# Performance work log

Measured on AMD Instinct MI355X. Metric: run time of the kernel, lower is better.

The kernel has to match this reference:

```python
import jax, jax.numpy as jnp
import numpy as np

B, T, S, L, R, H, UE = 64, 256, 16, 128, 16, 256, 64


def setup_inputs() -> dict:
    key = jax.random.key(0)
    ks = jax.random.split(key, 10)
    u = jax.random.normal(ks[0], (B, T, UE), jnp.float32)
    k = 0.1 * jax.random.normal(ks[1], (B, T, L), jnp.float32)
    K = 0.1 * jax.random.normal(ks[2], (B, T, L, R), jnp.float32)
    eps_z = jax.random.normal(ks[3], (T, S, B, L), jnp.float32)
    eps_w = jax.random.normal(ks[4], (T, S, B, R), jnp.float32)
    W1 = jax.random.normal(ks[5], (L, H), jnp.float32) / np.sqrt(L).astype(np.float32)
    W2 = jax.random.normal(ks[6], (H, L), jnp.float32) / np.sqrt(H).astype(np.float32)
    m_init = jax.random.normal(ks[7], (L,), jnp.float32)
    Q_diag = jax.random.uniform(ks[8], (L,), jnp.float32, 0.1, 1.0)
    Q0_diag = jax.random.uniform(ks[9], (L,), jnp.float32, 0.5, 1.5)
    return dict(u=u, k=k, K=K, eps_z=eps_z, eps_w=eps_w, W1=W1, W2=W2,
                m_init=m_init, Q_diag=Q_diag, Q0_diag=Q0_diag, n_samples=S)


def reference(u, k, K, eps_z, eps_w, W1, W2, m_init, Q_diag, Q0_diag, n_samples):
    Bn, Tn, Ln, Rn = K.shape
    ue = u.shape[-1]
    I_r = jnp.eye(Rn, dtype=K.dtype)

    def bmv(A, x):      # A: [B,L,R], x: [...,B,R] -> [...,B,L]
        return jnp.einsum('blr,...br->...bl', A, x)

    def bmvT(A, x):     # A: [B,L,R], x: [...,B,L] -> [...,B,R]
        return jnp.einsum('blr,...bl->...br', A, x)

    def mean_fn(z):
        return z + jnp.tanh(z @ W1) @ W2

    def step_core(m, K_t, k_t, ez, ew, q_a):
        # A = I + K^T diag(q_a) K  (rank x rank)
        A = I_r + jnp.einsum('blr,l,blq->brq', K_t, q_a, K_t)
        Lc = jnp.linalg.cholesky(A)
        Linv = jax.scipy.linalg.solve_triangular(
            Lc, jnp.broadcast_to(I_r, Lc.shape), lower=True)

        def csolve(x):  # solve A y = x via Linv^T Linv x
            y = jnp.einsum('bij,...bj->...bi', Linv, x)
            return jnp.einsum('bji,...bj->...bi', Linv, y)

        # gain direction; inner shift always uses Q_diag (as in torch source)
        g = k_t - bmv(K_t, csolve(bmvT(K_t, m + Q_diag * k_t)))
        m_f = m + q_a * g
        z_p = jnp.sqrt(q_a) * ez
        z_f = m_f + z_p - bmv(K_t, csolve(bmvT(K_t, z_p) + ew))
        qp = jnp.sum(q_a * g * g, axis=-1)
        M = A - I_r  # = K^T diag(q_a) K
        tr = -jnp.einsum('bij,bjk,bik->b', Linv, M, Linv)
        logdet = 2.0 * jnp.sum(jnp.log(jnp.diagonal(Lc, axis1=-2, axis2=-1)), axis=-1)
        kl = 0.5 * (qp + tr + logdet)
        return z_f, m_f, z_p, kl

    # ---- t = 0 (uses initial covariance Q0_diag) ----
    m0 = jnp.broadcast_to(m_init, (Bn, Ln))
    m0 = m0.at[:, :ue].add(u[:, 0])
    z_f0, m_f0, z_p0, kl0 = step_core(m0, K[:, 0], k[:, 0], eps_z[0], eps_w[0], Q0_diag)

    # ---- t = 1..T-1: sequential nonlinear filter scan ----
    def scan_fn(z_prev, xs):
        u_t, k_t, K_t, ez, ew = xs
        m = mean_fn(z_prev)            # [S,B,L]
        m = m.at[..., :ue].add(u_t)    # broadcast input over samples
        z_f, m_f, z_p, kl = step_core(m, K_t, k_t, ez, ew, Q_diag)
        return z_f, (z_f, m_f.mean(axis=0), z_p, kl.mean(axis=0))

    xs = (jnp.swapaxes(u[:, 1:], 0, 1),
          jnp.swapaxes(k[:, 1:], 0, 1),
          jnp.swapaxes(K[:, 1:], 0, 1),
          eps_z[1:], eps_w[1:])
    _, (z_fs, m_fs, z_ps, kls) = jax.lax.scan(scan_fn, z_f0, xs)

    z_f = jnp.transpose(jnp.concatenate([z_f0[None], z_fs], 0), (1, 2, 0, 3))  # [S,B,T,L]
    m_f = jnp.transpose(jnp.concatenate([m_f0[None], m_fs], 0), (1, 0, 2))     # [B,T,L]
    z_p = jnp.transpose(jnp.concatenate([z_p0[None], z_ps], 0), (1, 2, 0, 3))  # [S,B,T,L]
    kl = jnp.concatenate([kl0[None], kls], 0).T                                 # [B,T]
    return z_f, m_f, z_p, kl
```

## Files before the change

### kernel.cpp

```cpp
#include <hip/hip_runtime.h>
#include <cstddef>

typedef _Float16 half8v __attribute__((ext_vector_type(8)));
typedef _Float16 half4v __attribute__((ext_vector_type(4)));
typedef float f32x4 __attribute__((ext_vector_type(4)));

#define MFMA32(A, B, C) __builtin_amdgcn_mfma_f32_16x16x32_f16(A, B, C, 0, 0, 0)
#define MFMA16(A, B, C) __builtin_amdgcn_mfma_f32_16x16x16f16(A, B, C, 0, 0, 0)

__global__ void kw2_kernel(const float* __restrict__ W2, _Float16* __restrict__ w2h) {
  int i = blockIdx.x * 256 + threadIdx.x;
  w2h[i] = (_Float16)W2[i];
}

__global__ void kprep1_kernel(const float* __restrict__ Kg,
                              const float* __restrict__ kg,
                              const float* __restrict__ ug,
                              const float* __restrict__ Qd,
                              const float* __restrict__ Q0d,
                              float* __restrict__ Ainv,
                              float* __restrict__ klc,
                              _Float16* __restrict__ pfb,
                              float* __restrict__ cgp) {
  int tid = threadIdx.x;
  int wv = tid >> 6, ln = tid & 63;
  size_t bt = (size_t)blockIdx.x * 4 + wv;
  int t = (int)(bt & 255);
  __shared__ float Ks[4][128][20];
  __shared__ float qs[4][128];
  __shared__ float vvs[4][128];
  __shared__ float Asm[4][16][20];
  __shared__ float LiL[4][16][20];
  __shared__ float AiS[4][16][20];
  __shared__ float yps[4][4][16];
  __shared__ float yvs[4][16];

  const float* kp = Kg + bt * 2048;
  for (int i = ln; i < 2048; i += 64) Ks[wv][i >> 4][i & 15] = kp[i];
  for (int l = ln; l < 128; l += 64) {
    float q = (t == 0) ? Q0d[l] : Qd[l];
    qs[wv][l] = q;
    float v = Qd[l] * kg[bt * 128 + l];
    if (t > 0 && l < 64) v += ug[bt * 64 + l];
    vvs[wv][l] = v;
  }
  __syncthreads();
  {
    int r = ln & 15, c0 = (ln >> 4) << 2;
    float a0 = 0, a1 = 0, a2 = 0, a3 = 0;
    for (int l = 0; l < 128; ++l) {
      float kq = Ks[wv][l][r] * qs[wv][l];
      const float* row = &Ks[wv][l][c0];
      a0 += kq * row[0]; a1 += kq * row[1]; a2 += kq * row[2]; a3 += kq * row[3];
    }
    Asm[wv][r][c0 + 0] = a0 + ((r == c0 + 0) ? 1.f : 0.f);
    Asm[wv][r][c0 + 1] = a1 + ((r == c0 + 1) ? 1.f : 0.f);
    Asm[wv][r][c0 + 2] = a2 + ((r == c0 + 2) ? 1.f : 0.f);
    Asm[wv][r][c0 + 3] = a3 + ((r == c0 + 3) ? 1.f : 0.f);
  }
  {
    int r = ln & 15, seg = ln >> 4;
    float s = 0.f;
    for (int l = seg * 32; l < seg * 32 + 32; ++l) s += Ks[wv][l][r] * vvs[wv][l];
    yps[wv][seg][r] = s;
  }
  __syncthreads();
  if (ln < 16) {
    int i = ln;
    float ar[16], Lr[16];
#pragma unroll
    for (int j = 0; j < 16; ++j) ar[j] = Asm[wv][i][j];
    float ld = 0.f;
#pragma unroll
    for (int j = 0; j < 16; ++j) {
      float ajj = __shfl(ar[j], j, 64);
      float d = sqrtf(ajj);
      ld += __logf(d);
      float li = ar[j] / d;
      li = (i >= j) ? li : 0.f;
      Lr[j] = li;
#pragma unroll
      for (int k2 = j; k2 < 16; ++k2) {
        float lk = __shfl(li, k2, 64);
        ar[k2] -= li * lk;
      }
    }
    int cc = i;
    float Lic[16];
#pragma unroll
    for (int ii = 0; ii < 16; ++ii) {
      float s = (ii == cc) ? 1.f : 0.f;
#pragma unroll
      for (int p = 0; p < 16; ++p) {
        if (p < ii) {
          float Lip = __shfl(Lr[p], ii, 64);
          s -= Lip * Lic[p];
        }
      }
      float dii = __shfl(Lr[ii], ii, 64);
      float v = s / dii;
      Lic[ii] = (ii >= cc) ? v : 0.f;
    }
    float tr = 0.f;
#pragma unroll
    for (int ii = 0; ii < 16; ++ii) { tr += Lic[ii] * Lic[ii]; LiL[wv][cc][ii] = Lic[ii]; }
    tr += __shfl_xor(tr, 1); tr += __shfl_xor(tr, 2);
    tr += __shfl_xor(tr, 4); tr += __shfl_xor(tr, 8);
    if (cc == 0) klc[bt] = 0.5f * (tr - 16.f + 2.f * ld);
    yvs[wv][cc] = yps[wv][0][cc] + yps[wv][1][cc] + yps[wv][2][cc] + yps[wv][3][cc];
  }
  __syncthreads();
  {
    int r = ln & 15, c0 = (ln >> 4) << 2;
    float a0 = 0, a1 = 0, a2 = 0, a3 = 0;
    for (int ii = 0; ii < 16; ++ii) {
      float lir = LiL[wv][r][ii];
      a0 += lir * LiL[wv][c0 + 0][ii];
      a1 += lir * LiL[wv][c0 + 1][ii];
      a2 += lir * LiL[wv][c0 + 2][ii];
      a3 += lir * LiL[wv][c0 + 3][ii];
    }
    AiS[wv][r][c0 + 0] = a0; AiS[wv][r][c0 + 1] = a1;
    AiS[wv][r][c0 + 2] = a2; AiS[wv][r][c0 + 3] = a3;
    f32x4 av = {a0, a1, a2, a3};
    *(f32x4*)&Ainv[bt * 256 + r * 16 + c0] = av;
  }
  __syncthreads();
  {
#pragma unroll
    for (int li = 0; li < 2; ++li) {
      int l = ln * 2 + li;
      f32x4 acc0 = {0,0,0,0}, acc1v = {0,0,0,0}, acc2v = {0,0,0,0}, acc3v = {0,0,0,0};
      for (int j = 0; j < 16; ++j) {
        float kj = Ks[wv][l][j];
        acc0  += kj * *(const f32x4*)&AiS[wv][j][0];
        acc1v += kj * *(const f32x4*)&AiS[wv][j][4];
        acc2v += kj * *(const f32x4*)&AiS[wv][j][8];
        acc3v += kj * *(const f32x4*)&AiS[wv][j][12];
      }
      float ql = qs[wv][l];
      float cp = ql * kg[bt * 128 + l];
      float pv[16];
#pragma unroll
      for (int e = 0; e < 4; ++e) {
        pv[e] = ql * acc0[e]; pv[4 + e] = ql * acc1v[e];
        pv[8 + e] = ql * acc2v[e]; pv[12 + e] = ql * acc3v[e];
      }
#pragma unroll
      for (int r = 0; r < 16; ++r) cp -= pv[r] * yvs[wv][r];
      cgp[bt * 128 + l] = cp;
#pragma unroll
      for (int r = 0; r < 16; ++r) Ks[wv][l][r] = pv[r];
    }
  }
  __syncthreads();
  {
    int gp = ln >> 4, cp = ln & 15;
#pragma unroll
    for (int ci = 0; ci < 4; ++ci) {
      half8v o;
#pragma unroll
      for (int mt = 0; mt < 2; ++mt)
#pragma unroll
        for (int j = 0; j < 4; ++j)
          o[mt * 4 + j] = (_Float16)Ks[wv][ci * 32 + mt * 16 + cp][gp * 4 + j];
      *(half8v*)(pfb + bt * 2048 + (size_t)(ci * 64 + ln) * 8) = o;
    }
  }
}

__global__ void kprepR_kernel(const float* __restrict__ Kg,
                              const _Float16* __restrict__ w2h,
                              _Float16* __restrict__ rfb,
                              _Float16* __restrict__ kab) {
  int tid = threadIdx.x;
  int wv = tid >> 6, ln = tid & 63;
  int g = ln >> 4, c = ln & 15;
  __shared__ _Float16 Kh[128][20];
  __shared__ _Float16 Rh[16][264];
  for (int it = 0; it < 4; ++it) {
    size_t bt = (size_t)blockIdx.x * 4 + it;
    const float* kp = Kg + bt * 2048;
    for (int i = tid; i < 2048; i += 256) Kh[i >> 4][i & 15] = (_Float16)kp[i];
    __syncthreads();
    half8v kA[4];
#pragma unroll
    for (int kt = 0; kt < 4; ++kt)
#pragma unroll
      for (int j = 0; j < 8; ++j) kA[kt][j] = Kh[kt * 32 + g * 8 + j][c];
#pragma unroll
    for (int i = 0; i < 4; ++i) {
      int tile = wv * 4 + i;
      f32x4 acc = {0, 0, 0, 0};
#pragma unroll
      for (int kt = 0; kt < 4; ++kt) {
        half8v bf = *(const half8v*)&w2h[(size_t)(tile * 16 + c) * 128 + kt * 32 + g * 8];
        acc = MFMA32(kA[kt], bf, acc);
      }
#pragma unroll
      for (int r = 0; r < 4; ++r) Rh[g * 4 + r][tile * 16 + c] = (_Float16)acc[r];
    }
    __syncthreads();
    half8v r0, r1;
#pragma unroll
    for (int mt = 0; mt < 4; ++mt)
#pragma unroll
      for (int j = 0; j < 4; ++j) {
        _Float16 v = Rh[c][wv * 64 + mt * 16 + g * 4 + j];
        if (mt < 2) r0[mt * 4 + j] = v; else r1[(mt - 2) * 4 + j] = v;
      }
    *(half8v*)(rfb + bt * 4096 + (size_t)tid * 16) = r0;
    *(half8v*)(rfb + bt * 4096 + (size_t)tid * 16 + 8) = r1;
    if (kab) {
      half8v ko;
#pragma unroll
      for (int kt = 0; kt < 2; ++kt)
#pragma unroll
        for (int j = 0; j < 4; ++j) ko[kt * 4 + j] = Kh[wv * 32 + kt * 16 + g * 4 + j][c];
      *(half8v*)(kab + bt * 2048 + (size_t)tid * 8) = ko;
    }
    __syncthreads();
  }
}

__global__ void kc_kernel(const float* __restrict__ Kg,
                          const float* __restrict__ epsz,
                          const float* __restrict__ epsw,
                          const float* __restrict__ Qd,
                          const float* __restrict__ Q0d,
                          const float* __restrict__ Ainv,
                          float* __restrict__ out_zf,
                          float* __restrict__ out_zp,
                          float* __restrict__ zpcb,
                          int zw, int wzp) {
  int idx = blockIdx.x;
  int t = idx >> 6, b = idx & 63;
  int bt = b * 256 + t;
  __shared__ float Ks[128][16];
  __shared__ float Ai[16][16];
  __shared__ float zp[16][129];
  __shared__ float hh[16][17];
  __shared__ float ww[16][17];
  __shared__ float sq[128];
  const float* kp = Kg + (size_t)bt * 2048;
  for (int i = threadIdx.x; i < 2048; i += 256) ((float*)Ks)[i] = kp[i];
  ((float*)Ai)[threadIdx.x] = Ainv[(size_t)bt * 256 + threadIdx.x];
  const float* q = (t == 0) ? Q0d : Qd;
  if (threadIdx.x < 128) sq[threadIdx.x] = sqrtf(q[threadIdx.x]);
  __syncthreads();
  for (int i = threadIdx.x; i < 2048; i += 256) {
    int s = i >> 7, l = i & 127;
    float v = sq[l] * epsz[(((size_t)t * 16 + s) * 64 + b) * 128 + l];
    zp[s][l] = v;
    if (wzp) out_zp[(((size_t)s * 64 + b) * 256 + t) * 128 + l] = v;
  }
  __syncthreads();
  {
    int s = threadIdx.x >> 4, r = threadIdx.x & 15;
    float acc = epsw[(((size_t)t * 16 + s) * 64 + b) * 16 + r];
    for (int l = 0; l < 128; ++l) acc += Ks[l][r] * zp[s][l];
    hh[s][r] = acc;
  }
  __syncthreads();
  {
    int s = threadIdx.x >> 4, r = threadIdx.x & 15;
    float acc = 0.f;
    for (int j = 0; j < 16; ++j) acc += Ai[r][j] * hh[s][j];
    ww[s][r] = acc;
  }
  __syncthreads();
  for (int i = threadIdx.x; i < 2048; i += 256) {
    int s = i >> 7, l = i & 127;
    float acc = 0.f;
    for (int r = 0; r < 16; ++r) acc += Ks[l][r] * ww[s][r];
    float v = zp[s][l] - acc;
    if (zw) zpcb[(size_t)bt * 2048 + i] = v;
    else out_zf[(((size_t)s * 64 + b) * 256 + t) * 128 + l] = v;
  }
}

__global__ void kzp_kernel(const float* __restrict__ epsz,
                           const float* __restrict__ Qd,
                           const float* __restrict__ Q0d,
                           float* __restrict__ out_zp) {
  for (size_t i = (size_t)blockIdx.x * blockDim.x + threadIdx.x; i < (size_t)33554432;
       i += (size_t)gridDim.x * blockDim.x) {
    int l = (int)(i & 127);
    int t = (int)((i >> 7) & 255);
    int sb = (int)(i >> 15);
    int s = sb >> 6, b = sb & 63;
    float q = (t == 0) ? Q0d[l] : Qd[l];
    out_zp[i] = sqrtf(q) * epsz[(((size_t)t * 16 + s) * 64 + b) * 128 + l];
  }
}

#define BAR() asm volatile("s_waitcnt lgkmcnt(0)\n\ts_barrier" ::: "memory")

template <bool PK, bool ZW>
__device__ __forceinline__ void scan_body(
    const int b, const int ct,
    _Float16* __restrict__ svhc, _Float16* __restrict__ hbc,
    float (*__restrict__ h2pc)[320], float (*__restrict__ qppc)[64],
    const float* __restrict__ ug, const float* __restrict__ Kg,
    const float* __restrict__ W1, const float* __restrict__ W2,
    const float* __restrict__ m_init, const float* __restrict__ Qd,
    const float* __restrict__ Q0d, const _Float16* __restrict__ pfb,
    const float* __restrict__ cgp, const _Float16* __restrict__ rfb,
    const _Float16* __restrict__ kab, const float* __restrict__ zpcb,
    const float* __restrict__ klcp, float* __restrict__ out_zf,
    float* __restrict__ out_mf, float* __restrict__ out_kl) {
  const int wvc = ct >> 6;
  const int ln = ct & 63;
  const int g = ln >> 4;
  const int c = ln & 15;

  half8v w1f[4][4];
#pragma unroll
  for (int mt = 0; mt < 4; ++mt)
#pragma unroll
    for (int kt = 0; kt < 4; ++kt) {
      half8v v;
#pragma unroll
      for (int j = 0; j < 8; ++j)
        v[j] = (_Float16)W1[(size_t)(kt * 32 + g * 8 + j) * 256 + (wvc * 64 + mt * 16 + c)];
      w1f[mt][kt] = v;
    }
  half8v w2f[2][8];
#pragma unroll
  for (int mt = 0; mt < 2; ++mt)
#pragma unroll
    for (int kt = 0; kt < 8; ++kt) {
      half8v v;
#pragma unroll
      for (int j = 0; j < 8; ++j)
        v[j] = (_Float16)W2[(size_t)(kt * 32 + g * 8 + j) * 128 + (wvc * 32 + mt * 16 + c)];
      w2f[mt][kt] = v;
    }

  f32x4 qiv[2], qiv0[2];
#pragma unroll
  for (int mt = 0; mt < 2; ++mt) {
    f32x4 q = *(const f32x4*)&Qd[wvc * 32 + mt * 16 + g * 4];
    f32x4 q0 = *(const f32x4*)&Q0d[wvc * 32 + mt * 16 + g * 4];
#pragma unroll
    for (int r = 0; r < 4; ++r) { qiv[mt][r] = 1.f / q[r]; qiv0[mt][r] = 1.f / q0[r]; }
  }

  f32x4 zreg[2];

  half8v pfx0, pfx1, kax0 = {}, kax1 = {}, rfa0, rfa1, rfc0, rfc1;
  float kf0[8], kf1[8];
  f32x4 zq0[2], zq1[2], cv0[2], cv1[2];
  f32x4 ur0[2] = {}, ur1[2] = {};
  float kv0 = 0.f, kv1 = 0.f;

  const char* pf_p = (const char*)pfb + (size_t)b * 256 * 4096 + (size_t)ct * 16;
  const char* ka_p = PK ? (const char*)kab + (size_t)b * 256 * 4096 + (size_t)ct * 16
                        : (const char*)pfb;
  const char* K_p = (const char*)Kg + (size_t)b * 256 * 8192 + (size_t)((wvc * 32 + g * 4) * 16 + c) * 4;
  const char* rf_p = (const char*)rfb + (size_t)b * 256 * 8192 + (size_t)ct * 32;
  const char* zq_p = ZW ? (const char*)zpcb + (size_t)b * 256 * 8192 + (size_t)(c * 128 + wvc * 32 + g * 4) * 4
                        : (const char*)out_zf + ((((size_t)c * 64 + b) * 256) * 128 + wvc * 32 + g * 4) * 4;
  const size_t zq_str = ZW ? 8192 : 512;
  const char* cv_p = (const char*)cgp + (size_t)b * 256 * 512 + (size_t)(wvc * 32 + g * 4) * 4;
  const char* ur_p = (const char*)ug + (size_t)b * 256 * 256 + (size_t)(wvc * 32 + g * 4) * 4;
  const char* kl_p = (const char*)klcp + (size_t)b * 256 * 4;
  char* zf_p = (char*)out_zf + ((((size_t)c * 64 + b) * 256) * 128 + wvc * 32 + g * 4) * 4;
  char* mf_p = (char*)out_mf + ((size_t)b * 256 * 128 + wvc * 32 + g * 4) * 4;

#define STAGE(BI) do { \
    pfx##BI = *(const half8v*)pf_p; pf_p += 4096; \
    if constexpr (PK) { kax##BI = *(const half8v*)ka_p; ka_p += 4096; } \
    else { _Pragma("unroll") for (int kt_ = 0; kt_ < 2; ++kt_) \
             _Pragma("unroll") for (int j_ = 0; j_ < 4; ++j_) \
               kf##BI[kt_ * 4 + j_] = *(const float*)(K_p + kt_ * 1024 + j_ * 64); \
           K_p += 8192; } \
    rfa##BI = *(const half8v*)rf_p; rfc##BI = *(const half8v*)(rf_p + 16); rf_p += 8192; \
    zq##BI[0] = *(const f32x4*)zq_p; zq##BI[1] = *(const f32x4*)(zq_p + 64); zq_p += zq_str; \
    cv##BI[0] = *(const f32x4*)cv_p; cv##BI[1] = *(const f32x4*)(cv_p + 64); cv_p += 512; \
    if (wvc < 2) { ur##BI[0] = *(const f32x4*)ur_p; ur##BI[1] = *(const f32x4*)(ur_p + 64); } \
    ur_p += 256; \
    kv##BI = *(const float*)kl_p; kl_p += 4; \
  } while (0)

#define KAH(BI, KT, DST) do { \
    if constexpr (PK) { _Pragma("unroll") for (int j_ = 0; j_ < 4; ++j_) DST[j_] = kax##BI[(KT) * 4 + j_]; } \
    else { _Pragma("unroll") for (int j_ = 0; j_ < 4; ++j_) DST[j_] = (_Float16)kf##BI[(KT) * 4 + j_]; } \
  } while (0)

#define PHASE_A(BI) do { \
    half4v zbh_[2], zbl_[2]; \
    _Pragma("unroll") for (int kt = 0; kt < 2; ++kt) \
      _Pragma("unroll") for (int j = 0; j < 4; ++j) { \
        float x_ = zreg[kt][j]; _Float16 h_ = (_Float16)x_; \
        zbh_[kt][j] = h_; zbl_[kt][j] = (_Float16)(x_ - (float)h_); } \
    half8v zh8_[4]; \
    _Pragma("unroll") for (int kt = 0; kt < 4; ++kt) { \
      int row_ = kt * 4 + g; \
      int idx_ = row_ * 128 + (((c + row_) & 15) << 3); \
      zh8_[kt] = *(const half8v*)&svhc[idx_]; } \
    f32x4 a1h_[4]; \
    _Pragma("unroll") for (int mt = 0; mt < 4; ++mt) a1h_[mt] = (f32x4){0,0,0,0}; \
    _Pragma("unroll") for (int kt = 0; kt < 4; ++kt) \
      _Pragma("unroll") for (int mt = 0; mt < 4; ++mt) \
        a1h_[mt] = MFMA32(w1f[mt][kt], zh8_[kt], a1h_[mt]); \
    half4v th_[4]; \
    _Pragma("unroll") for (int mt = 0; mt < 4; ++mt) { \
      _Pragma("unroll") for (int r = 0; r < 4; ++r) { \
        float x_ = a1h_[mt][r]; \
        float e_ = __expf(2.f * x_); \
        th_[mt][r] = (_Float16)(1.f - 2.f / (e_ + 1.f)); } \
      int row_ = wvc * 8 + mt * 2 + (g >> 1); \
      *(half4v*)&hbc[row_ * 128 + (((c + row_) & 15) << 3) + ((g & 1) << 2)] = th_[mt]; } \
    half4v ka0_, ka1_; KAH(BI, 0, ka0_); KAH(BI, 1, ka1_); \
    f32x4 hz_ = {0, 0, 0, 0}; \
    hz_ = MFMA16(ka0_, zbh_[0], hz_); hz_ = MFMA16(ka1_, zbh_[1], hz_); \
    hz_ = MFMA16(ka0_, zbl_[0], hz_); hz_ = MFMA16(ka1_, zbl_[1], hz_); \
    f32x4 hr_ = {0, 0, 0, 0}; \
    _Pragma("unroll") for (int mt = 0; mt < 4; ++mt) { \
      half4v rr_; \
      _Pragma("unroll") for (int j = 0; j < 4; ++j) \
        rr_[j] = (mt < 2) ? rfa##BI[mt * 4 + j] : rfc##BI[(mt - 2) * 4 + j]; \
      hr_ = MFMA16(rr_, th_[mt], hr_); } \
    *(f32x4*)&h2pc[wvc][c * 20 + g * 4] = hz_ + hr_; \
  } while (0)

#define EPILOG(BI, QIV, MV) do { \
    f32x4 h2v_ = *(const f32x4*)&h2pc[0][c * 20 + g * 4]; \
    h2v_ += *(const f32x4*)&h2pc[1][c * 20 + g * 4]; \
    h2v_ += *(const f32x4*)&h2pc[2][c * 20 + g * 4]; \
    h2v_ += *(const f32x4*)&h2pc[3][c * 20 + g * 4]; \
    half4v h2h_, h2l_; \
    _Pragma("unroll") for (int j = 0; j < 4; ++j) { \
      _Float16 h_ = (_Float16)h2v_[j]; \
      h2h_[j] = h_; h2l_[j] = (_Float16)(h2v_[j] - (float)h_); } \
    float qpl_ = 0.f; \
    _Pragma("unroll") for (int mt = 0; mt < 2; ++mt) { \
      half4v pfm_; \
      _Pragma("unroll") for (int j = 0; j < 4; ++j) pfm_[j] = pfx##BI[mt * 4 + j]; \
      f32x4 zz_ = {0, 0, 0, 0}; \
      f32x4 mh_ = MFMA16(pfm_, h2h_, zz_); \
      f32x4 mlv_ = MFMA16(pfm_, h2l_, zz_); \
      f32x4 dd_ = cv##BI[mt] - (mh_ + mlv_); \
      f32x4 mf_ = MV[mt] + dd_; \
      f32x4 zf_ = mf_ + zq##BI[mt]; \
      _Pragma("unroll") for (int r = 0; r < 4; ++r) qpl_ += dd_[r] * dd_[r] * QIV[mt][r]; \
      *(f32x4*)(zf_p + mt * 64) = zf_; \
      zreg[mt] = zf_; \
      half4v zh4_; \
      _Pragma("unroll") for (int r = 0; r < 4; ++r) zh4_[r] = (_Float16)zf_[r]; \
      int row_ = wvc * 4 + mt * 2 + (g >> 1); \
      int base_ = row_ * 128 + (((c + row_) & 15) << 3) + ((g & 1) << 2); \
      *(half4v*)&svhc[base_] = zh4_; \
      f32x4 ms_ = mf_; \
      _Pragma("unroll") for (int r = 0; r < 4; ++r) { \
        float x_ = ms_[r]; \
        x_ += __shfl_xor(x_, 1); x_ += __shfl_xor(x_, 2); \
        x_ += __shfl_xor(x_, 4); x_ += __shfl_xor(x_, 8); \
        ms_[r] = x_ * 0.0625f; } \
      if (c == 0) *(f32x4*)(mf_p + mt * 64) = ms_; \
    } \
    zf_p += 512; mf_p += 512; \
    qpl_ += __shfl_xor(qpl_, 16); \
    qpl_ += __shfl_xor(qpl_, 32); \
    if (g == 0) qppc[BI][wvc * 16 + c] = qpl_; \
  } while (0)

#define PHASE_B(BI, QIV) do { \
    half8v hf_[8]; \
    _Pragma("unroll") for (int kt = 0; kt < 8; ++kt) { \
      int row_ = kt * 4 + g; \
      hf_[kt] = *(const half8v*)&hbc[row_ * 128 + (((c + row_) & 15) << 3)]; } \
    f32x4 a2a_[2], a2b_[2]; \
    _Pragma("unroll") for (int mt = 0; mt < 2; ++mt) { a2a_[mt] = (f32x4){0,0,0,0}; a2b_[mt] = (f32x4){0,0,0,0}; } \
    _Pragma("unroll") for (int kt = 0; kt < 4; ++kt) \
      _Pragma("unroll") for (int mt = 0; mt < 2; ++mt) { \
        a2a_[mt] = MFMA32(w2f[mt][kt], hf_[kt], a2a_[mt]); \
        a2b_[mt] = MFMA32(w2f[mt][kt + 4], hf_[kt + 4], a2b_[mt]); } \
    f32x4 mv_[2]; \
    _Pragma("unroll") for (int mt = 0; mt < 2; ++mt) { \
      mv_[mt] = zreg[mt] + a2a_[mt] + a2b_[mt]; \
      if (wvc < 2) mv_[mt] += ur##BI[mt]; } \
    EPILOG(BI, QIV, mv_); \
  } while (0)

#define KL_FIN(PBI, TPREV) do { \
    if (ct < 16) { \
      float v_ = qppc[PBI][ct] + qppc[PBI][16 + ct] + qppc[PBI][32 + ct] + qppc[PBI][48 + ct]; \
      v_ += __shfl_xor(v_, 1); v_ += __shfl_xor(v_, 2); \
      v_ += __shfl_xor(v_, 4); v_ += __shfl_xor(v_, 8); \
      if (ct == 0) out_kl[(size_t)b * 256 + (size_t)(TPREV)] = 0.03125f * v_ + kv##PBI; \
    } \
  } while (0)

  STAGE(0);
  STAGE(1);
  {
    f32x4 mv0[2];
#pragma unroll
    for (int mt = 0; mt < 2; ++mt) {
      mv0[mt] = *(const f32x4*)&m_init[wvc * 32 + mt * 16 + g * 4];
      if (wvc < 2) mv0[mt] += ur0[mt];
    }
    half4v mh0[2], ml0[2];
#pragma unroll
    for (int kt = 0; kt < 2; ++kt)
#pragma unroll
      for (int j = 0; j < 4; ++j) {
        float x = mv0[kt][j];
        _Float16 h = (_Float16)x;
        mh0[kt][j] = h;
        ml0[kt][j] = (_Float16)(x - (float)h);
      }
    half4v ka0_, ka1_;
    KAH(0, 0, ka0_); KAH(0, 1, ka1_);
    f32x4 hz = {0, 0, 0, 0};
    hz = MFMA16(ka0_, mh0[0], hz); hz = MFMA16(ka1_, mh0[1], hz);
    hz = MFMA16(ka0_, ml0[0], hz); hz = MFMA16(ka1_, ml0[1], hz);
    *(f32x4*)&h2pc[wvc][c * 20 + g * 4] = hz;
    BAR();
    EPILOG(0, qiv0, mv0);
    BAR();
  }

  for (int t = 1; t < 255; t += 2) {
    KL_FIN(0, t - 1);
    STAGE(0);
    PHASE_A(1);
    BAR();
    PHASE_B(1, qiv);
    BAR();
    KL_FIN(1, t);
    STAGE(1);
    PHASE_A(0);
    BAR();
    PHASE_B(0, qiv);
    BAR();
  }
  KL_FIN(0, 254);
  PHASE_A(1);
  BAR();
  PHASE_B(1, qiv);
  BAR();
  KL_FIN(1, 255);

#undef STAGE
#undef KAH
#undef PHASE_A
#undef EPILOG
#undef PHASE_B
#undef KL_FIN
}

template <bool PK, bool ZW>
__launch_bounds__(256, 1)
__global__ void kscan1_kernel(const float* __restrict__ ug, const float* __restrict__ Kg,
                              const float* __restrict__ W1, const float* __restrict__ W2,
                              const float* __restrict__ m_init, const float* __restrict__ Qd,
                              const float* __restrict__ Q0d, const _Float16* __restrict__ pfb,
                              const float* __restrict__ cgp, const _Float16* __restrict__ rfb,
                              const _Float16* __restrict__ kab, const float* __restrict__ zpcb,
                              const float* __restrict__ klcp, float* __restrict__ out_zf,
                              float* __restrict__ out_mf, float* __restrict__ out_kl) {
  __shared__ __align__(16) _Float16 svh[2048];
  __shared__ __align__(16) _Float16 hb[4096];
  __shared__ float h2p[4][320];
  __shared__ float qpp[2][64];
  scan_body<PK, ZW>(blockIdx.x, threadIdx.x, svh, hb, h2p, qpp,
                    ug, Kg, W1, W2, m_init, Qd, Q0d, pfb, cgp, rfb, kab, zpcb, klcp,
                    out_zf, out_mf, out_kl);
}

template <bool PK, bool ZW>
__attribute__((amdgpu_flat_work_group_size(512, 512)))
__attribute__((amdgpu_waves_per_eu(2, 2)))
__global__ void kscan2_kernel(const float* __restrict__ ug, const float* __restrict__ Kg,
                              const float* __restrict__ W1, const float* __restrict__ W2,
                              const float* __restrict__ m_init, const float* __restrict__ Qd,
                              const float* __restrict__ Q0d, const _Float16* __restrict__ pfb,
                              const float* __restrict__ cgp, const _Float16* __restrict__ rfb,
                              const _Float16* __restrict__ kab, const float* __restrict__ zpcb,
                              const float* __restrict__ klcp, float* __restrict__ out_zf,
                              float* __restrict__ out_mf, float* __restrict__ out_kl) {
  __shared__ __align__(16) _Float16 svh[2][2048];
  __shared__ __align__(16) _Float16 hb[2][4096];
  __shared__ float h2p[2][4][320];
  __shared__ float qpp[2][2][64];
  const int ch = threadIdx.x >> 8;
  scan_body<PK, ZW>(blockIdx.x * 2 + ch, threadIdx.x & 255,
                    svh[ch], hb[ch], h2p[ch], qpp[ch],
                    ug, Kg, W1, W2, m_init, Qd, Q0d, pfb, cgp, rfb, kab, zpcb, klcp,
                    out_zf, out_mf, out_kl);
}

extern "C" void kernel_launch(void* const* d_in, const int* in_sizes, int n_in,
                              void* d_out, int out_size, void* d_ws, size_t ws_size,
                              hipStream_t stream) {
  (void)in_sizes; (void)n_in; (void)out_size;
  const float* u   = (const float*)d_in[0];
  const float* kk  = (const float*)d_in[1];
  const float* Kg  = (const float*)d_in[2];
  const float* epz = (const float*)d_in[3];
  const float* epw = (const float*)d_in[4];
  const float* W1  = (const float*)d_in[5];
  const float* W2  = (const float*)d_in[6];
  const float* mi  = (const float*)d_in[7];
  const float* Qd  = (const float*)d_in[8];
  const float* Q0d = (const float*)d_in[9];

  float* out_zf = (float*)d_out;
  float* out_mf = out_zf + (size_t)33554432;
  float* out_zp = out_mf + (size_t)2097152;
  float* out_kl = out_zp + (size_t)33554432;

  char* ws = (char*)d_ws;
  size_t off = 0;
  auto take = [&](size_t n) { char* p = ws + off; off += n; return p; };
  float*    Ainv = (float*)take(16777216);
  float*    klc  = (float*)take(65536);
  float*    cgp  = (float*)take(8388608);
  _Float16* pfb  = (_Float16*)take(67108864);
  _Float16* w2h  = (_Float16*)take(65536);
  bool zw = ws_size >= off + 134217728;
  float* zpcb = zw ? (float*)take(134217728) : nullptr;
  bool pk = zw && (ws_size >= off + 67108864);
  _Float16* kab = pk ? (_Float16*)take(67108864) : nullptr;
  bool rfws = ws_size >= off + 134217728;
  _Float16* rfb = rfws ? (_Float16*)take(134217728) : (_Float16*)out_zp;
  int wzp = rfws ? 1 : 0;

  kw2_kernel<<<128, 256, 0, stream>>>(W2, w2h);
  kprep1_kernel<<<4096, 256, 0, stream>>>(Kg, kk, u, Qd, Q0d, Ainv, klc, pfb, cgp);
  kprepR_kernel<<<4096, 256, 0, stream>>>(Kg, w2h, rfb, kab);
  kc_kernel<<<16384, 256, 0, stream>>>(Kg, epz, epw, Qd, Q0d, Ainv, out_zf, out_zp,
                                       zpcb, zw ? 1 : 0, wzp);

  auto pick = [&](const void* f2) {
    hipFuncAttributes fa;
    if (hipFuncGetAttributes(&fa, f2) == hipSuccess)
      return fa.localSizeBytes == 0 && fa.numRegs > 140;
    return false;
  };
#define LAUNCH_SCAN(PKV, ZWV) do { \
    if (pick((const void*)kscan2_kernel<PKV, ZWV>)) \
      kscan2_kernel<PKV, ZWV><<<32, 512, 0, stream>>>(u, Kg, W1, W2, mi, Qd, Q0d, pfb, cgp, rfb, kab, zpcb, klc, out_zf, out_mf, out_kl); \
    else \
      kscan1_kernel<PKV, ZWV><<<64, 256, 0, stream>>>(u, Kg, W1, W2, mi, Qd, Q0d, pfb, cgp, rfb, kab, zpcb, klc, out_zf, out_mf, out_kl); \
  } while (0)

  if (pk)      LAUNCH_SCAN(true,  true);
  else if (zw) LAUNCH_SCAN(false, true);
  else         LAUNCH_SCAN(false, false);
#undef LAUNCH_SCAN

  if (!rfws) kzp_kernel<<<2048, 256, 0, stream>>>(epz, Qd, Q0d, out_zp);
}
```

Measured before the change: 1.078 ms.

## Fuse prep stages and scan into one persistent kernel with per-timestep flags

Merges the precompute kernels (Cholesky/inverse, W2 projection, noise correction, z_p output) into a single launch. In it, 64 blocks run the sequential scan while 192 worker blocks produce per-(b,t) data and signal readiness through global flags. Scan blocks spin on acquire loads before consuming each timestep, so preprocessing overlaps the latency-bound scan instead of running before it. This relies on all 256 blocks being co-resident, since otherwise the spin-waits could deadlock. It also drops the two-chain-per-block scan variant.

```diff
diff --git a/kernel.cpp b/kernel.cpp
--- a/kernel.cpp
+++ b/kernel.cpp
@@ -11,287 +11,6 @@
 __global__ void kw2_kernel(const float* __restrict__ W2, _Float16* __restrict__ w2h) {
   int i = blockIdx.x * 256 + threadIdx.x;
   w2h[i] = (_Float16)W2[i];
-}
-
-__global__ void kprep1_kernel(const float* __restrict__ Kg,
-                              const float* __restrict__ kg,
-                              const float* __restrict__ ug,
-                              const float* __restrict__ Qd,
-                              const float* __restrict__ Q0d,
-                              float* __restrict__ Ainv,
-                              float* __restrict__ klc,
-                              _Float16* __restrict__ pfb,
-                              float* __restrict__ cgp) {
-  int tid = threadIdx.x;
-  int wv = tid >> 6, ln = tid & 63;
-  size_t bt = (size_t)blockIdx.x * 4 + wv;
-  int t = (int)(bt & 255);
-  __shared__ float Ks[4][128][20];
-  __shared__ float qs[4][128];
-  __shared__ float vvs[4][128];
-  __shared__ float Asm[4][16][20];
-  __shared__ float LiL[4][16][20];
-  __shared__ float AiS[4][16][20];
-  __shared__ float yps[4][4][16];
-  __shared__ float yvs[4][16];
-
-  const float* kp = Kg + bt * 2048;
-  for (int i = ln; i < 2048; i += 64) Ks[wv][i >> 4][i & 15] = kp[i];
-  for (int l = ln; l < 128; l += 64) {
-    float q = (t == 0) ? Q0d[l] : Qd[l];
-    qs[wv][l] = q;
-    float v = Qd[l] * kg[bt * 128 + l];
-    if (t > 0 && l < 64) v += ug[bt * 64 + l];
-    vvs[wv][l] = v;
-  }
-  __syncthreads();
-  {
-    int r = ln & 15, c0 = (ln >> 4) << 2;
-    float a0 = 0, a1 = 0, a2 = 0, a3 = 0;
-    for (int l = 0; l < 128; ++l) {
-      float kq = Ks[wv][l][r] * qs[wv][l];
-      const float* row = &Ks[wv][l][c0];
-      a0 += kq * row[0]; a1 += kq * row[1]; a2 += kq * row[2]; a3 += kq * row[3];
-    }
-    Asm[wv][r][c0 + 0] = a0 + ((r == c0 + 0) ? 1.f : 0.f);
-    Asm[wv][r][c0 + 1] = a1 + ((r == c0 + 1) ? 1.f : 0.f);
-    Asm[wv][r][c0 + 2] = a2 + ((r == c0 + 2) ? 1.f : 0.f);
-    Asm[wv][r][c0 + 3] = a3 + ((r == c0 + 3) ? 1.f : 0.f);
-  }
-  {
-    int r = ln & 15, seg = ln >> 4;
-    float s = 0.f;
-    for (int l = seg * 32; l < seg * 32 + 32; ++l) s += Ks[wv][l][r] * vvs[wv][l];
-    yps[wv][seg][r] = s;
-  }
-  __syncthreads();
-  if (ln < 16) {
-    int i = ln;
-    float ar[16], Lr[16];
-#pragma unroll
-    for (int j = 0; j < 16; ++j) ar[j] = Asm[wv][i][j];
-    float ld = 0.f;
-#pragma unroll
-    for (int j = 0; j < 16; ++j) {
-      float ajj = __shfl(ar[j], j, 64);
-      float d = sqrtf(ajj);
-      ld += __logf(d);
-      float li = ar[j] / d;
-      li = (i >= j) ? li : 0.f;
-      Lr[j] = li;
-#pragma unroll
-      for (int k2 = j; k2 < 16; ++k2) {
-        float lk = __shfl(li, k2, 64);
-        ar[k2] -= li * lk;
-      }
-    }
-    int cc = i;
-    float Lic[16];
-#pragma unroll
-    for (int ii = 0; ii < 16; ++ii) {
-      float s = (ii == cc) ? 1.f : 0.f;
-#pragma unroll
-      for (int p = 0; p < 16; ++p) {
-        if (p < ii) {
-          float Lip = __shfl(Lr[p], ii, 64);
-          s -= Lip * Lic[p];
-        }
-      }
-      float dii = __shfl(Lr[ii], ii, 64);
-      float v = s / dii;
-      Lic[ii] = (ii >= cc) ? v : 0.f;
-    }
-    float tr = 0.f;
-#pragma unroll
-    for (int ii = 0; ii < 16; ++ii) { tr += Lic[ii] * Lic[ii]; LiL[wv][cc][ii] = Lic[ii]; }
-    tr += __shfl_xor(tr, 1); tr += __shfl_xor(tr, 2);
-    tr += __shfl_xor(tr, 4); tr += __shfl_xor(tr, 8);
-    if (cc == 0) klc[bt] = 0.5f * (tr - 16.f + 2.f * ld);
-    yvs[wv][cc] = yps[wv][0][cc] + yps[wv][1][cc] + yps[wv][2][cc] + yps[wv][3][cc];
-  }
-  __syncthreads();
-  {
-    int r = ln & 15, c0 = (ln >> 4) << 2;
-    float a0 = 0, a1 = 0, a2 = 0, a3 = 0;
-    for (int ii = 0; ii < 16; ++ii) {
-      float lir = LiL[wv][r][ii];
-      a0 += lir * LiL[wv][c0 + 0][ii];
-      a1 += lir * LiL[wv][c0 + 1][ii];
-      a2 += lir * LiL[wv][c0 + 2][ii];
-      a3 += lir * LiL[wv][c0 + 3][ii];
-    }
-    AiS[wv][r][c0 + 0] = a0; AiS[wv][r][c0 + 1] = a1;
-    AiS[wv][r][c0 + 2] = a2; AiS[wv][r][c0 + 3] = a3;
-    f32x4 av = {a0, a1, a2, a3};
-    *(f32x4*)&Ainv[bt * 256 + r * 16 + c0] = av;
-  }
-  __syncthreads();
-  {
-#pragma unroll
-    for (int li = 0; li < 2; ++li) {
-      int l = ln * 2 + li;
-      f32x4 acc0 = {0,0,0,0}, acc1v = {0,0,0,0}, acc2v = {0,0,0,0}, acc3v = {0,0,0,0};
-      for (int j = 0; j < 16; ++j) {
-        float kj = Ks[wv][l][j];
-        acc0  += kj * *(const f32x4*)&AiS[wv][j][0];
-        acc1v += kj * *(const f32x4*)&AiS[wv][j][4];
-        acc2v += kj * *(const f32x4*)&AiS[wv][j][8];
-        acc3v += kj * *(const f32x4*)&AiS[wv][j][12];
-      }
-      float ql = qs[wv][l];
-      float cp = ql * kg[bt * 128 + l];
-      float pv[16];
-#pragma unroll
-      for (int e = 0; e < 4; ++e) {
-        pv[e] = ql * acc0[e]; pv[4 + e] = ql * acc1v[e];
-        pv[8 + e] = ql * acc2v[e]; pv[12 + e] = ql * acc3v[e];
-      }
-#pragma unroll
-      for (int r = 0; r < 16; ++r) cp -= pv[r] * yvs[wv][r];
-      cgp[bt * 128 + l] = cp;
-#pragma unroll
-      for (int r = 0; r < 16; ++r) Ks[wv][l][r] = pv[r];
-    }
-  }
-  __syncthreads();
-  {
-    int gp = ln >> 4, cp = ln & 15;
-#pragma unroll
-    for (int ci = 0; ci < 4; ++ci) {
-      half8v o;
-#pragma unroll
-      for (int mt = 0; mt < 2; ++mt)
-#pragma unroll
-        for (int j = 0; j < 4; ++j)
-          o[mt * 4 + j] = (_Float16)Ks[wv][ci * 32 + mt * 16 + cp][gp * 4 + j];
-      *(half8v*)(pfb + bt * 2048 + (size_t)(ci * 64 + ln) * 8) = o;
-    }
-  }
-}
-
-__global__ void kprepR_kernel(const float* __restrict__ Kg,
-                              const _Float16* __restrict__ w2h,
-                              _Float16* __restrict__ rfb,
-                              _Float16* __restrict__ kab) {
-  int tid = threadIdx.x;
-  int wv = tid >> 6, ln = tid & 63;
-  int g = ln >> 4, c = ln & 15;
-  __shared__ _Float16 Kh[128][20];
-  __shared__ _Float16 Rh[16][264];
-  for (int it = 0; it < 4; ++it) {
-    size_t bt = (size_t)blockIdx.x * 4 + it;
-    const float* kp = Kg + bt * 2048;
-    for (int i = tid; i < 2048; i += 256) Kh[i >> 4][i & 15] = (_Float16)kp[i];
-    __syncthreads();
-    half8v kA[4];
-#pragma unroll
-    for (int kt = 0; kt < 4; ++kt)
-#pragma unroll
-      for (int j = 0; j < 8; ++j) kA[kt][j] = Kh[kt * 32 + g * 8 + j][c];
-#pragma unroll
-    for (int i = 0; i < 4; ++i) {
-      int tile = wv * 4 + i;
-      f32x4 acc = {0, 0, 0, 0};
-#pragma unroll
-      for (int kt = 0; kt < 4; ++kt) {
-        half8v bf = *(const half8v*)&w2h[(size_t)(tile * 16 + c) * 128 + kt * 32 + g * 8];
-        acc = MFMA32(kA[kt], bf, acc);
-      }
-#pragma unroll
-      for (int r = 0; r < 4; ++r) Rh[g * 4 + r][tile * 16 + c] = (_Float16)acc[r];
-    }
-    __syncthreads();
-    half8v r0, r1;
-#pragma unroll
-    for (int mt = 0; mt < 4; ++mt)
-#pragma unroll
-      for (int j = 0; j < 4; ++j) {
-        _Float16 v = Rh[c][wv * 64 + mt * 16 + g * 4 + j];
-        if (mt < 2) r0[mt * 4 + j] = v; else r1[(mt - 2) * 4 + j] = v;
-      }
-    *(half8v*)(rfb + bt * 4096 + (size_t)tid * 16) = r0;
-    *(half8v*)(rfb + bt * 4096 + (size_t)tid * 16 + 8) = r1;
-    if (kab) {
-      half8v ko;
-#pragma unroll
-      for (int kt = 0; kt < 2; ++kt)
-#pragma unroll
-        for (int j = 0; j < 4; ++j) ko[kt * 4 + j] = Kh[wv * 32 + kt * 16 + g * 4 + j][c];
-      *(half8v*)(kab + bt * 2048 + (size_t)tid * 8) = ko;
-    }
-    __syncthreads();
-  }
-}
-
-__global__ void kc_kernel(const float* __restrict__ Kg,
-                          const float* __restrict__ epsz,
-                          const float* __restrict__ epsw,
-                          const float* __restrict__ Qd,
-                          const float* __restrict__ Q0d,
-                          const float* __restrict__ Ainv,
-                          float* __restrict__ out_zf,
-                          float* __restrict__ out_zp,
-                          float* __restrict__ zpcb,
-                          int zw, int wzp) {
-  int idx = blockIdx.x;
-  int t = idx >> 6, b = idx & 63;
-  int bt = b * 256 + t;
-  __shared__ float Ks[128][16];
-  __shared__ float Ai[16][16];
-  __shared__ float zp[16][129];
-  __shared__ float hh[16][17];
-  __shared__ float ww[16][17];
-  __shared__ float sq[128];
-  const float* kp = Kg + (size_t)bt * 2048;
-  for (int i = threadIdx.x; i < 2048; i += 256) ((float*)Ks)[i] = kp[i];
-  ((float*)Ai)[threadIdx.x] = Ainv[(size_t)bt * 256 + threadIdx.x];
-  const float* q = (t == 0) ? Q0d : Qd;
-  if (threadIdx.x < 128) sq[threadIdx.x] = sqrtf(q[threadIdx.x]);
-  __syncthreads();
-  for (int i = threadIdx.x; i < 2048; i += 256) {
-    int s = i >> 7, l = i & 127;
-    float v = sq[l] * epsz[(((size_t)t * 16 + s) * 64 + b) * 128 + l];
-    zp[s][l] = v;
-    if (wzp) out_zp[(((size_t)s * 64 + b) * 256 + t) * 128 + l] = v;
-  }
-  __syncthreads();
-  {
-    int s = threadIdx.x >> 4, r = threadIdx.x & 15;
-    float acc = epsw[(((size_t)t * 16 + s) * 64 + b) * 16 + r];
-    for (int l = 0; l < 128; ++l) acc += Ks[l][r] * zp[s][l];
-    hh[s][r] = acc;
-  }
-  __syncthreads();
-  {
-    int s = threadIdx.x >> 4, r = threadIdx.x & 15;
-    float acc = 0.f;
-    for (int j = 0; j < 16; ++j) acc += Ai[r][j] * hh[s][j];
-    ww[s][r] = acc;
-  }
-  __syncthreads();
-  for (int i = threadIdx.x; i < 2048; i += 256) {
-    int s = i >> 7, l = i & 127;
-    float acc = 0.f;
-    for (int r = 0; r < 16; ++r) acc += Ks[l][r] * ww[s][r];
-    float v = zp[s][l] - acc;
-    if (zw) zpcb[(size_t)bt * 2048 + i] = v;
-    else out_zf[(((size_t)s * 64 + b) * 256 + t) * 128 + l] = v;
-  }
-}
-
-__global__ void kzp_kernel(const float* __restrict__ epsz,
-                           const float* __restrict__ Qd,
-                           const float* __restrict__ Q0d,
-                           float* __restrict__ out_zp) {
-  for (size_t i = (size_t)blockIdx.x * blockDim.x + threadIdx.x; i < (size_t)33554432;
-       i += (size_t)gridDim.x * blockDim.x) {
-    int l = (int)(i & 127);
-    int t = (int)((i >> 7) & 255);
-    int sb = (int)(i >> 15);
-    int s = sb >> 6, b = sb & 63;
-    float q = (t == 0) ? Q0d[l] : Qd[l];
-    out_zp[i] = sqrtf(q) * epsz[(((size_t)t * 16 + s) * 64 + b) * 128 + l];
-  }
 }
 
 #define BAR() asm volatile("s_waitcnt lgkmcnt(0)\n\ts_barrier" ::: "memory")
@@ -308,11 +27,17 @@
     const float* __restrict__ cgp, const _Float16* __restrict__ rfb,
     const _Float16* __restrict__ kab, const float* __restrict__ zpcb,
     const float* __restrict__ klcp, float* __restrict__ out_zf,
-    float* __restrict__ out_mf, float* __restrict__ out_kl) {
+    float* __restrict__ out_mf, float* __restrict__ out_kl,
+    unsigned* flags) {
   const int wvc = ct >> 6;
   const int ln = ct & 63;
   const int g = ln >> 4;
   const int c = ln & 15;
+
+#define WAITF(T) do { if (flags) { \
+    unsigned* fp_ = flags + ((size_t)b * 256 + (size_t)(T)); \
+    while (__hip_atomic_load(fp_, __ATOMIC_ACQUIRE, __HIP_MEMORY_SCOPE_AGENT) == 0u) \
+      __builtin_amdgcn_s_sleep(8); } } while (0)
 
   half8v w1f[4][4];
 #pragma unroll
@@ -493,7 +218,9 @@
     } \
   } while (0)
 
+  WAITF(0);
   STAGE(0);
+  WAITF(1);
   STAGE(1);
   {
     f32x4 mv0[2];
@@ -525,12 +252,14 @@
 
   for (int t = 1; t < 255; t += 2) {
     KL_FIN(0, t - 1);
+    WAITF(t + 1);
     STAGE(0);
     PHASE_A(1);
     BAR();
     PHASE_B(1, qiv);
     BAR();
     KL_FIN(1, t);
+    WAITF(t + 2);
     STAGE(1);
     PHASE_A(0);
     BAR();
@@ -550,6 +279,7 @@
 #undef EPILOG
 #undef PHASE_B
 #undef KL_FIN
+#undef WAITF
 }
 
 template <bool PK, bool ZW>
@@ -568,29 +298,521 @@
   __shared__ float qpp[2][64];
   scan_body<PK, ZW>(blockIdx.x, threadIdx.x, svh, hb, h2p, qpp,
                     ug, Kg, W1, W2, m_init, Qd, Q0d, pfb, cgp, rfb, kab, zpcb, klcp,
-                    out_zf, out_mf, out_kl);
+                    out_zf, out_mf, out_kl, nullptr);
 }
 
-template <bool PK, bool ZW>
-__attribute__((amdgpu_flat_work_group_size(512, 512)))
-__attribute__((amdgpu_waves_per_eu(2, 2)))
-__global__ void kscan2_kernel(const float* __restrict__ ug, const float* __restrict__ Kg,
-                              const float* __restrict__ W1, const float* __restrict__ W2,
-                              const float* __restrict__ m_init, const float* __restrict__ Qd,
-                              const float* __restrict__ Q0d, const _Float16* __restrict__ pfb,
-                              const float* __restrict__ cgp, const _Float16* __restrict__ rfb,
-                              const _Float16* __restrict__ kab, const float* __restrict__ zpcb,
-                              const float* __restrict__ klcp, float* __restrict__ out_zf,
-                              float* __restrict__ out_mf, float* __restrict__ out_kl) {
-  __shared__ __align__(16) _Float16 svh[2][2048];
-  __shared__ __align__(16) _Float16 hb[2][4096];
-  __shared__ float h2p[2][4][320];
-  __shared__ float qpp[2][2][64];
-  const int ch = threadIdx.x >> 8;
-  scan_body<PK, ZW>(blockIdx.x * 2 + ch, threadIdx.x & 255,
-                    svh[ch], hb[ch], h2p[ch], qpp[ch],
-                    ug, Kg, W1, W2, m_init, Qd, Q0d, pfb, cgp, rfb, kab, zpcb, klcp,
-                    out_zf, out_mf, out_kl);
+__launch_bounds__(256, 1)
+__global__ void fused_kernel(const float* __restrict__ ug, const float* __restrict__ kg,
+                             const float* __restrict__ Kg, const float* __restrict__ epz,
+                             const float* __restrict__ epw, const float* __restrict__ W1,
+                             const float* __restrict__ W2, const float* __restrict__ m_init,
+                             const float* __restrict__ Qd, const float* __restrict__ Q0d,
+                             const _Float16* __restrict__ w2h,
+                             _Float16* __restrict__ pfb, float* __restrict__ cgp,
+                             _Float16* __restrict__ rfb, _Float16* __restrict__ kab,
+                             float* __restrict__ zpcb, float* __restrict__ klc,
+                             unsigned* __restrict__ flags,
+                             float* __restrict__ out_zf, float* __restrict__ out_mf,
+                             float* __restrict__ out_zp, float* __restrict__ out_kl) {
+  __shared__ __align__(16) char raw[42240];
+  const int tid = threadIdx.x;
+
+  if (blockIdx.x < 64) {
+    _Float16* svh = (_Float16*)raw;
+    _Float16* hb = (_Float16*)(raw + 4096);
+    float (*h2p)[320] = (float (*)[320])(raw + 12288);
+    float (*qpp)[64] = (float (*)[64])(raw + 17408);
+    scan_body<true, true>(blockIdx.x, tid, svh, hb, h2p, qpp,
+                          ug, Kg, W1, W2, m_init, Qd, Q0d, pfb, cgp, rfb, kab,
+                          zpcb, klc, out_zf, out_mf, out_kl, flags);
+    return;
+  }
+
+  float (*Ks)[17] = (float (*)[17])raw;
+  float* qs = (float*)(raw + 8704);
+  float* kvv = (float*)(raw + 9216);
+  float* sq = (float*)(raw + 9728);
+  float (*Asm)[17] = (float (*)[17])(raw + 10240);
+  float (*LiL)[17] = (float (*)[17])(raw + 11328);
+  float (*AiS)[17] = (float (*)[17])(raw + 12416);
+  float (*yps)[16] = (float (*)[16])(raw + 13504);
+  float* yvs = (float*)(raw + 14528);
+  float (*zp)[129] = (float (*)[129])(raw + 14592);
+  float (*hh)[17] = (float (*)[17])(raw + 22848);
+  float (*ww)[17] = (float (*)[17])(raw + 23936);
+  _Float16 (*Rh)[264] = (_Float16 (*)[264])(raw + 25024);
+  float (*Ps)[17] = (float (*)[17])(raw + 33472);
+  float* vvs = (float*)ww;
+
+  const int wv = tid >> 6;
+  const int g = (tid >> 4) & 3;
+  const int c = tid & 15;
+
+  for (int item = (int)blockIdx.x - 64; item < 16384; item += 192) {
+    const int t = item >> 6, b = item & 63;
+    const size_t bt = (size_t)b * 256 + t;
+    const float* kp = Kg + bt * 2048;
+    for (int i = tid; i < 2048; i += 256) Ks[i >> 4][i & 15] = kp[i];
+    if (tid < 128) {
+      float q = (t == 0) ? Q0d[tid] : Qd[tid];
+      qs[tid] = q;
+      sq[tid] = sqrtf(q);
+      float kvl = kg[bt * 128 + tid];
+      kvv[tid] = kvl;
+      float v = Qd[tid] * kvl;
+      if (t > 0 && tid < 64) v += ug[bt * 64 + tid];
+      vvs[tid] = v;
+    }
+    __syncthreads();
+    {
+      int r = tid & 15, c2 = tid >> 4;
+      float a = 0.f;
+      for (int l = 0; l < 128; ++l) a += Ks[l][r] * qs[l] * Ks[l][c2];
+      Asm[r][c2] = a + ((r == c2) ? 1.f : 0.f);
+    }
+    {
+      int seg = tid >> 4, r = tid & 15;
+      float s = 0.f;
+      for (int l = seg * 8; l < seg * 8 + 8; ++l) s += Ks[l][r] * vvs[l];
+      yps[seg][r] = s;
+    }
+    for (int i = tid; i < 2048; i += 256) {
+      int s = i >> 7, l = i & 127;
+      float v = sq[l] * epz[(((size_t)t * 16 + s) * 64 + b) * 128 + l];
+      zp[s][l] = v;
+      out_zp[(((size_t)s * 64 + b) * 256 + t) * 128 + l] = v;
+    }
+    {
+      half8v kA[4];
+#pragma unroll
+      for (int kt = 0; kt < 4; ++kt)
+#pragma unroll
+        for (int j = 0; j < 8; ++j) kA[kt][j] = (_Float16)Ks[kt * 32 + g * 8 + j][c];
+#pragma unroll
+      for (int i = 0; i < 4; ++i) {
+        int tile = wv * 4 + i;
+        f32x4 acc = {0, 0, 0, 0};
+#pragma unroll
+        for (int kt = 0; kt < 4; ++kt) {
+          half8v bf = *(const half8v*)&w2h[(size_t)(tile * 16 + c) * 128 + kt * 32 + g * 8];
+          acc = MFMA32(kA[kt], bf, acc);
+        }
+#pragma unroll
+        for (int r = 0; r < 4; ++r) Rh[g * 4 + r][tile * 16 + c] = (_Float16)acc[r];
+      }
+    }
+    __syncthreads();
+    if (tid < 64) {
+      if (tid < 16) {
+        int i = tid;
+        float ar[16], Lr[16];
+#pragma unroll
+        for (int j = 0; j < 16; ++j) ar[j] = Asm[i][j];
+        float ld = 0.f;
+#pragma unroll
+        for (int j = 0; j < 16; ++j) {
+          float ajj = __shfl(ar[j], j, 64);
+          float d = sqrtf(ajj);
+          ld += __logf(d);
+          float li = ar[j] / d;
+          li = (i >= j) ? li : 0.f;
+          Lr[j] = li;
+#pragma unroll
+          for (int k2 = j; k2 < 16; ++k2) {
+            float lk = __shfl(li, k2, 64);
+            ar[k2] -= li * lk;
+          }
+        }
+        int cc = i;
+        float Lic[16];
+#pragma unroll
+        for (int ii = 0; ii < 16; ++ii) {
+          float s = (ii == cc) ? 1.f : 0.f;
+#pragma unroll
+          for (int p = 0; p < 16; ++p) {
+            if (p < ii) {
+              float Lip = __shfl(Lr[p], ii, 64);
+              s -= Lip * Lic[p];
+            }
+          }
+          float dii = __shfl(Lr[ii], ii, 64);
+          float v = s / dii;
+          Lic[ii] = (ii >= cc) ? v : 0.f;
+        }
+        float tr = 0.f;
+#pragma unroll
+        for (int ii = 0; ii < 16; ++ii) { tr += Lic[ii] * Lic[ii]; LiL[cc][ii] = Lic[ii]; }
+        tr += __shfl_xor(tr, 1); tr += __shfl_xor(tr, 2);
+        tr += __shfl_xor(tr, 4); tr += __shfl_xor(tr, 8);
+        if (cc == 0) klc[bt] = 0.5f * (tr - 16.f + 2.f * ld);
+        float yv = 0.f;
+#pragma unroll
+        for (int seg = 0; seg < 16; ++seg) yv += yps[seg][cc];
+        yvs[cc] = yv;
+      }
+    } else {
+      half8v r0, r1;
+#pragma unroll
+      for (int mt = 0; mt < 4; ++mt)
+#pragma unroll
+        for (int j = 0; j < 4; ++j) {
+          _Float16 v = Rh[c][wv * 64 + mt * 16 + g * 4 + j];
+          if (mt < 2) r0[mt * 4 + j] = v; else r1[(mt - 2) * 4 + j] = v;
+        }
+      *(half8v*)(rfb + bt * 4096 + (size_t)tid * 16) = r0;
+      *(half8v*)(rfb + bt * 4096 + (size_t)tid * 16 + 8) = r1;
+      half8v ko;
+#pragma unroll
+      for (int kt = 0; kt < 2; ++kt)
+#pragma unroll
+        for (int j = 0; j < 4; ++j) ko[kt * 4 + j] = (_Float16)Ks[wv * 32 + kt * 16 + g * 4 + j][c];
+      *(half8v*)(kab + bt * 2048 + (size_t)tid * 8) = ko;
+    }
+    __syncthreads();
+    {
+      int r = tid & 15, c2 = tid >> 4;
+      float a = 0.f;
+      for (int ii = 0; ii < 16; ++ii) a += LiL[r][ii] * LiL[c2][ii];
+      AiS[r][c2] = a;
+    }
+    {
+      int s = tid >> 4, r = tid & 15;
+      float acc = epw[(((size_t)t * 16 + s) * 64 + b) * 16 + r];
+      for (int l = 0; l < 128; ++l) acc += Ks[l][r] * zp[s][l];
+      hh[s][r] = acc;
+    }
+    if (tid < 64) {
+      half8v r0, r1;
+#pragma unroll
+      for (int mt = 0; mt < 4; ++mt)
+#pragma unroll
+        for (int j = 0; j < 4; ++j) {
+          _Float16 v = Rh[c][mt * 16 + g * 4 + j];
+          if (mt < 2) r0[mt * 4 + j] = v; else r1[(mt - 2) * 4 + j] = v;
+        }
+      *(half8v*)(rfb + bt * 4096 + (size_t)tid * 16) = r0;
+      *(half8v*)(rfb + bt * 4096 + (size_t)tid * 16 + 8) = r1;
+      half8v ko;
+#pragma unroll
+      for (int kt = 0; kt < 2; ++kt)
+#pragma unroll
+        for (int j = 0; j < 4; ++j) ko[kt * 4 + j] = (_Float16)Ks[kt * 16 + g * 4 + j][c];
+      *(half8v*)(kab + bt * 2048 + (size_t)tid * 8) = ko;
+    }
+    __syncthreads();
+    {
+      int l = tid >> 1, r0c = (tid & 1) * 8;
+      float pr[8];
+#pragma unroll
+      for (int r = 0; r < 8; ++r) {
+        float s = 0.f;
+        for (int j = 0; j < 16; ++j) s += Ks[l][j] * AiS[j][r0c + r];
+        pr[r] = qs[l] * s;
+      }
+#pragma unroll
+      for (int r = 0; r < 8; ++r) Ps[l][r0c + r] = pr[r];
+    }
+    {
+      int s = tid >> 4, r = tid & 15;
+      float acc = 0.f;
+      for (int j = 0; j < 16; ++j) acc += AiS[r][j] * hh[s][j];
+      ww[s][r] = acc;
+    }
+    __syncthreads();
+    if (tid < 128) {
+      int l = tid;
+      float cp = qs[l] * kvv[l];
+      for (int r = 0; r < 16; ++r) cp -= Ps[l][r] * yvs[r];
+      cgp[bt * 128 + l] = cp;
+    }
+    for (int i = tid; i < 2048; i += 256) {
+      int s = i >> 7, l = i & 127;
+      float acc = 0.f;
+      for (int r = 0; r < 16; ++r) acc += Ks[l][r] * ww[s][r];
+      zpcb[bt * 2048 + i] = zp[s][l] - acc;
+    }
+    {
+      half8v o;
+#pragma unroll
+      for (int mt = 0; mt < 2; ++mt)
+#pragma unroll
+        for (int j = 0; j < 4; ++j)
+          o[mt * 4 + j] = (_Float16)Ps[wv * 32 + mt * 16 + c][g * 4 + j];
+      *(half8v*)(pfb + bt * 2048 + (size_t)tid * 8) = o;
+    }
+    __syncthreads();
+    if (tid == 0) {
+      __threadfence();
+      __hip_atomic_store(&flags[bt], 1u, __ATOMIC_RELEASE, __HIP_MEMORY_SCOPE_AGENT);
+    }
+  }
+}
+
+__global__ void kprep1_kernel(const float* __restrict__ Kg, const float* __restrict__ kg,
+                              const float* __restrict__ ug, const float* __restrict__ Qd,
+                              const float* __restrict__ Q0d, float* __restrict__ Ainv,
+                              float* __restrict__ klc, _Float16* __restrict__ pfb,
+                              float* __restrict__ cgp) {
+  int tid = threadIdx.x;
+  int wv = tid >> 6, ln = tid & 63;
+  size_t bt = (size_t)blockIdx.x * 4 + wv;
+  int t = (int)(bt & 255);
+  __shared__ float Ks[4][128][20];
+  __shared__ float qs[4][128];
+  __shared__ float vvs[4][128];
+  __shared__ float Asm[4][16][20];
+  __shared__ float LiL[4][16][20];
+  __shared__ float AiS[4][16][20];
+  __shared__ float yps[4][4][16];
+  __shared__ float yvs[4][16];
+  const float* kp = Kg + bt * 2048;
+  for (int i = ln; i < 2048; i += 64) Ks[wv][i >> 4][i & 15] = kp[i];
+  for (int l = ln; l < 128; l += 64) {
+    float q = (t == 0) ? Q0d[l] : Qd[l];
+    qs[wv][l] = q;
+    float v = Qd[l] * kg[bt * 128 + l];
+    if (t > 0 && l < 64) v += ug[bt * 64 + l];
+    vvs[wv][l] = v;
+  }
+  __syncthreads();
+  {
+    int r = ln & 15, c0 = (ln >> 4) << 2;
+    float a0 = 0, a1 = 0, a2 = 0, a3 = 0;
+    for (int l = 0; l < 128; ++l) {
+      float kq = Ks[wv][l][r] * qs[wv][l];
+      const float* row = &Ks[wv][l][c0];
+      a0 += kq * row[0]; a1 += kq * row[1]; a2 += kq * row[2]; a3 += kq * row[3];
+    }
+    Asm[wv][r][c0 + 0] = a0 + ((r == c0 + 0) ? 1.f : 0.f);
+    Asm[wv][r][c0 + 1] = a1 + ((r == c0 + 1) ? 1.f : 0.f);
+    Asm[wv][r][c0 + 2] = a2 + ((r == c0 + 2) ? 1.f : 0.f);
+    Asm[wv][r][c0 + 3] = a3 + ((r == c0 + 3) ? 1.f : 0.f);
+  }
+  {
+    int r = ln & 15, seg = ln >> 4;
+    float s = 0.f;
+    for (int l = seg * 32; l < seg * 32 + 32; ++l) s += Ks[wv][l][r] * vvs[wv][l];
+    yps[wv][seg][r] = s;
+  }
+  __syncthreads();
+  if (ln < 16) {
+    int i = ln;
+    float ar[16], Lr[16];
+#pragma unroll
+    for (int j = 0; j < 16; ++j) ar[j] = Asm[wv][i][j];
+    float ld = 0.f;
+#pragma unroll
+    for (int j = 0; j < 16; ++j) {
+      float ajj = __shfl(ar[j], j, 64);
+      float d = sqrtf(ajj);
+      ld += __logf(d);
+      float li = ar[j] / d;
+      li = (i >= j) ? li : 0.f;
+      Lr[j] = li;
+#pragma unroll
+      for (int k2 = j; k2 < 16; ++k2) {
+        float lk = __shfl(li, k2, 64);
+        ar[k2] -= li * lk;
+      }
+    }
+    int cc = i;
+    float Lic[16];
+#pragma unroll
+    for (int ii = 0; ii < 16; ++ii) {
+      float s = (ii == cc) ? 1.f : 0.f;
+#pragma unroll
+      for (int p = 0; p < 16; ++p) {
+        if (p < ii) {
+          float Lip = __shfl(Lr[p], ii, 64);
+          s -= Lip * Lic[p];
+        }
+      }
+      float dii = __shfl(Lr[ii], ii, 64);
+      float v = s / dii;
+      Lic[ii] = (ii >= cc) ? v : 0.f;
+    }
+    float tr = 0.f;
+#pragma unroll
+    for (int ii = 0; ii < 16; ++ii) { tr += Lic[ii] * Lic[ii]; LiL[wv][cc][ii] = Lic[ii]; }
+    tr += __shfl_xor(tr, 1); tr += __shfl_xor(tr, 2);
+    tr += __shfl_xor(tr, 4); tr += __shfl_xor(tr, 8);
+    if (cc == 0) klc[bt] = 0.5f * (tr - 16.f + 2.f * ld);
+    yvs[wv][cc] = yps[wv][0][cc] + yps[wv][1][cc] + yps[wv][2][cc] + yps[wv][3][cc];
+  }
+  __syncthreads();
+  {
+    int r = ln & 15, c0 = (ln >> 4) << 2;
+    float a0 = 0, a1 = 0, a2 = 0, a3 = 0;
+    for (int ii = 0; ii < 16; ++ii) {
+      float lir = LiL[wv][r][ii];
+      a0 += lir * LiL[wv][c0 + 0][ii];
+      a1 += lir * LiL[wv][c0 + 1][ii];
+      a2 += lir * LiL[wv][c0 + 2][ii];
+      a3 += lir * LiL[wv][c0 + 3][ii];
+    }
+    AiS[wv][r][c0 + 0] = a0; AiS[wv][r][c0 + 1] = a1;
+    AiS[wv][r][c0 + 2] = a2; AiS[wv][r][c0 + 3] = a3;
+    f32x4 av = {a0, a1, a2, a3};
+    *(f32x4*)&Ainv[bt * 256 + r * 16 + c0] = av;
+  }
+  __syncthreads();
+  {
+#pragma unroll
+    for (int li = 0; li < 2; ++li) {
+      int l = ln * 2 + li;
+      f32x4 acc0 = {0,0,0,0}, acc1v = {0,0,0,0}, acc2v = {0,0,0,0}, acc3v = {0,0,0,0};
+      for (int j = 0; j < 16; ++j) {
+        float kj = Ks[wv][l][j];
+        acc0  += kj * *(const f32x4*)&AiS[wv][j][0];
+        acc1v += kj * *(const f32x4*)&AiS[wv][j][4];
+        acc2v += kj * *(const f32x4*)&AiS[wv][j][8];
+        acc3v += kj * *(const f32x4*)&AiS[wv][j][12];
+      }
+      float ql = qs[wv][l];
+      float cp = ql * kg[bt * 128 + l];
+      float pv[16];
+#pragma unroll
+      for (int e = 0; e < 4; ++e) {
+        pv[e] = ql * acc0[e]; pv[4 + e] = ql * acc1v[e];
+        pv[8 + e] = ql * acc2v[e]; pv[12 + e] = ql * acc3v[e];
+      }
+#pragma unroll
+      for (int r = 0; r < 16; ++r) cp -= pv[r] * yvs[wv][r];
+      cgp[bt * 128 + l] = cp;
+#pragma unroll
+      for (int r = 0; r < 16; ++r) Ks[wv][l][r] = pv[r];
+    }
+  }
+  __syncthreads();
+  {
+    int gp = ln >> 4, cp = ln & 15;
+#pragma unroll
+    for (int ci = 0; ci < 4; ++ci) {
+      half8v o;
+#pragma unroll
+      for (int mt = 0; mt < 2; ++mt)
+#pragma unroll
+        for (int j = 0; j < 4; ++j)
+          o[mt * 4 + j] = (_Float16)Ks[wv][ci * 32 + mt * 16 + cp][gp * 4 + j];
+      *(half8v*)(pfb + bt * 2048 + (size_t)(ci * 64 + ln) * 8) = o;
+    }
+  }
+}
+
+__global__ void kprepR_kernel(const float* __restrict__ Kg, const _Float16* __restrict__ w2h,
+                              _Float16* __restrict__ rfb, _Float16* __restrict__ kab) {
+  int tid = threadIdx.x;
+  int wv = tid >> 6, ln = tid & 63;
+  int g = ln >> 4, c = ln & 15;
+  __shared__ _Float16 Kh[128][20];
+  __shared__ _Float16 Rh[16][264];
+  for (int it = 0; it < 4; ++it) {
+    size_t bt = (size_t)blockIdx.x * 4 + it;
+    const float* kp = Kg + bt * 2048;
+    for (int i = tid; i < 2048; i += 256) Kh[i >> 4][i & 15] = (_Float16)kp[i];
+    __syncthreads();
+    half8v kA[4];
+#pragma unroll
+    for (int kt = 0; kt < 4; ++kt)
+#pragma unroll
+      for (int j = 0; j < 8; ++j) kA[kt][j] = Kh[kt * 32 + g * 8 + j][c];
+#pragma unroll
+    for (int i = 0; i < 4; ++i) {
+      int tile = wv * 4 + i;
+      f32x4 acc = {0, 0, 0, 0};
+#pragma unroll
+      for (int kt = 0; kt < 4; ++kt) {
+        half8v bf = *(const half8v*)&w2h[(size_t)(tile * 16 + c) * 128 + kt * 32 + g * 8];
+        acc = MFMA32(kA[kt], bf, acc);
+      }
+#pragma unroll
+      for (int r = 0; r < 4; ++r) Rh[g * 4 + r][tile * 16 + c] = (_Float16)acc[r];
+    }
+    __syncthreads();
+    half8v r0, r1;
+#pragma unroll
+    for (int mt = 0; mt < 4; ++mt)
+#pragma unroll
+      for (int j = 0; j < 4; ++j) {
+        _Float16 v = Rh[c][wv * 64 + mt * 16 + g * 4 + j];
+        if (mt < 2) r0[mt * 4 + j] = v; else r1[(mt - 2) * 4 + j] = v;
+      }
+    *(half8v*)(rfb + bt * 4096 + (size_t)tid * 16) = r0;
+    *(half8v*)(rfb + bt * 4096 + (size_t)tid * 16 + 8) = r1;
+    if (kab) {
+      half8v ko;
+#pragma unroll
+      for (int kt = 0; kt < 2; ++kt)
+#pragma unroll
+        for (int j = 0; j < 4; ++j) ko[kt * 4 + j] = Kh[wv * 32 + kt * 16 + g * 4 + j][c];
+      *(half8v*)(kab + bt * 2048 + (size_t)tid * 8) = ko;
+    }
+    __syncthreads();
+  }
+}
+
+__global__ void kc_kernel(const float* __restrict__ Kg, const float* __restrict__ epsz,
+                          const float* __restrict__ epsw, const float* __restrict__ Qd,
+                          const float* __restrict__ Q0d, const float* __restrict__ Ainv,
+                          float* __restrict__ out_zf, float* __restrict__ out_zp,
+                          float* __restrict__ zpcb, int zw, int wzp) {
+  int idx = blockIdx.x;
+  int t = idx >> 6, b = idx & 63;
+  int bt = b * 256 + t;
+  __shared__ float Ks[128][16];
+  __shared__ float Ai[16][16];
+  __shared__ float zp[16][129];
+  __shared__ float hh[16][17];
+  __shared__ float ww[16][17];
+  __shared__ float sq[128];
+  const float* kp = Kg + (size_t)bt * 2048;
+  for (int i = threadIdx.x; i < 2048; i += 256) ((float*)Ks)[i] = kp[i];
+  ((float*)Ai)[threadIdx.x] = Ainv[(size_t)bt * 256 + threadIdx.x];
+  const float* q = (t == 0) ? Q0d : Qd;
+  if (threadIdx.x < 128) sq[threadIdx.x] = sqrtf(q[threadIdx.x]);
+  __syncthreads();
+  for (int i = threadIdx.x; i < 2048; i += 256) {
+    int s = i >> 7, l = i & 127;
+    float v = sq[l] * epsz[(((size_t)t * 16 + s) * 64 + b) * 128 + l];
+    zp[s][l] = v;
+    if (wzp) out_zp[(((size_t)s * 64 + b) * 256 + t) * 128 + l] = v;
+  }
+  __syncthreads();
+  {
+    int s = threadIdx.x >> 4, r = threadIdx.x & 15;
+    float acc = epsw[(((size_t)t * 16 + s) * 64 + b) * 16 + r];
+    for (int l = 0; l < 128; ++l) acc += Ks[l][r] * zp[s][l];
+    hh[s][r] = acc;
+  }
+  __syncthreads();
+  {
+    int s = threadIdx.x >> 4, r = threadIdx.x & 15;
+    float acc = 0.f;
+    for (int j = 0; j < 16; ++j) acc += Ai[r][j] * hh[s][j];
+    ww[s][r] = acc;
+  }
+  __syncthreads();
+  for (int i = threadIdx.x; i < 2048; i += 256) {
+    int s = i >> 7, l = i & 127;
+    float acc = 0.f;
+    for (int r = 0; r < 16; ++r) acc += Ks[l][r] * ww[s][r];
+    float v = zp[s][l] - acc;
+    if (zw) zpcb[(size_t)bt * 2048 + i] = v;
+    else out_zf[(((size_t)s * 64 + b) * 256 + t) * 128 + l] = v;
+  }
+}
+
+__global__ void kzp_kernel(const float* __restrict__ epsz, const float* __restrict__ Qd,
+                           const float* __restrict__ Q0d, float* __restrict__ out_zp) {
+  for (size_t i = (size_t)blockIdx.x * blockDim.x + threadIdx.x; i < (size_t)33554432;
+       i += (size_t)gridDim.x * blockDim.x) {
+    int l = (int)(i & 127);
+    int t = (int)((i >> 7) & 255);
+    int sb = (int)(i >> 15);
+    int s = sb >> 6, b = sb & 63;
+    float q = (t == 0) ? Q0d[l] : Qd[l];
+    out_zp[i] = sqrtf(q) * epsz[(((size_t)t * 16 + s) * 64 + b) * 128 + l];
+  }
 }
 
 extern "C" void kernel_launch(void* const* d_in, const int* in_sizes, int n_in,
@@ -614,6 +836,42 @@
   float* out_kl = out_zp + (size_t)33554432;
 
   char* ws = (char*)d_ws;
+
+  const size_t F_klc = 0;
+  const size_t F_cgp = 65536;
+  const size_t F_pfb = 8454144;
+  const size_t F_w2h = 75563008;
+  const size_t F_kab = 75628544;
+  const size_t F_rfb = 142737408;
+  const size_t F_zpc = 276955136;
+  const size_t F_flg = 411172864;
+  const size_t F_END = 411238400;
+
+  bool fuse = ws_size >= F_END;
+  if (fuse) {
+    hipFuncAttributes fa;
+    if (hipFuncGetAttributes(&fa, (const void*)fused_kernel) != hipSuccess ||
+        fa.localSizeBytes != 0)
+      fuse = false;
+  }
+
+  if (fuse) {
+    float*    klc  = (float*)(ws + F_klc);
+    float*    cgp  = (float*)(ws + F_cgp);
+    _Float16* pfb  = (_Float16*)(ws + F_pfb);
+    _Float16* w2h  = (_Float16*)(ws + F_w2h);
+    _Float16* kab  = (_Float16*)(ws + F_kab);
+    _Float16* rfb  = (_Float16*)(ws + F_rfb);
+    float*    zpcb = (float*)(ws + F_zpc);
+    unsigned* flags = (unsigned*)(ws + F_flg);
+    kw2_kernel<<<128, 256, 0, stream>>>(W2, w2h);
+    hipMemsetAsync(flags, 0, 65536, stream);
+    fused_kernel<<<256, 256, 0, stream>>>(u, kk, Kg, epz, epw, W1, W2, mi, Qd, Q0d,
+                                          w2h, pfb, cgp, rfb, kab, zpcb, klc, flags,
+                                          out_zf, out_mf, out_zp, out_kl);
+    return;
+  }
+
   size_t off = 0;
   auto take = [&](size_t n) { char* p = ws + off; off += n; return p; };
   float*    Ainv = (float*)take(16777216);
@@ -634,24 +892,11 @@
   kprepR_kernel<<<4096, 256, 0, stream>>>(Kg, w2h, rfb, kab);
   kc_kernel<<<16384, 256, 0, stream>>>(Kg, epz, epw, Qd, Q0d, Ainv, out_zf, out_zp,
                                        zpcb, zw ? 1 : 0, wzp);
-
-  auto pick = [&](const void* f2) {
-    hipFuncAttributes fa;
-    if (hipFuncGetAttributes(&fa, f2) == hipSuccess)
-      return fa.localSizeBytes == 0 && fa.numRegs > 140;
-    return false;
-  };
-#define LAUNCH_SCAN(PKV, ZWV) do { \
-    if (pick((const void*)kscan2_kernel<PKV, ZWV>)) \
-      kscan2_kernel<PKV, ZWV><<<32, 512, 0, stream>>>(u, Kg, W1, W2, mi, Qd, Q0d, pfb, cgp, rfb, kab, zpcb, klc, out_zf, out_mf, out_kl); \
-    else \
-      kscan1_kernel<PKV, ZWV><<<64, 256, 0, stream>>>(u, Kg, W1, W2, mi, Qd, Q0d, pfb, cgp, rfb, kab, zpcb, klc, out_zf, out_mf, out_kl); \
-  } while (0)
-
-  if (pk)      LAUNCH_SCAN(true,  true);
-  else if (zw) LAUNCH_SCAN(false, true);
-  else         LAUNCH_SCAN(false, false);
-#undef LAUNCH_SCAN
-
+  if (pk)
+    kscan1_kernel<true, true><<<64, 256, 0, stream>>>(u, Kg, W1, W2, mi, Qd, Q0d, pfb, cgp, rfb, kab, zpcb, klc, out_zf, out_mf, out_kl);
+  else if (zw)
+    kscan1_kernel<false, true><<<64, 256, 0, stream>>>(u, Kg, W1, W2, mi, Qd, Q0d, pfb, cgp, rfb, kab, zpcb, klc, out_zf, out_mf, out_kl);
+  else
+    kscan1_kernel<false, false><<<64, 256, 0, stream>>>(u, Kg, W1, W2, mi, Qd, Q0d, pfb, cgp, rfb, kab, zpcb, klc, out_zf, out_mf, out_kl);
   if (!rfws) kzp_kernel<<<2048, 256, 0, stream>>>(epz, Qd, Q0d, out_zp);
 }
```

Result: slower. 3.089 ms (+186.5%).
